# Performance work log

Hardware: AMD Instinct MI355X
Metric: run time of the kernel (lower is better)

The kernel has to match this reference:

```python
import jax, jax.numpy as jnp
import numpy as np

NP, NC, F, H = 50000, 10000, 128, 256
E_ANNO, E_LINK, E_PPI, NPAIR = 250000, 100000, 500000, 4096


def _sage(x_src, x_dst, src, dst, Wl, b, Wr):
    # PyG SAGEConv(aggr='mean'): lin_l(mean of gathered neighbor feats) + lin_r(x_dst)
    n_dst = x_dst.shape[0]
    agg = jax.ops.segment_sum(x_src[src], dst, num_segments=n_dst)
    cnt = jax.ops.segment_sum(jnp.ones((src.shape[0], 1), x_src.dtype), dst, num_segments=n_dst)
    mean = agg / jnp.maximum(cnt, 1.0)  # isolated dst nodes get 0
    return mean @ Wl.T + b + x_dst @ Wr.T


def setup_inputs():
    key = jax.random.key(0)
    ks = iter(jax.random.split(key, 64))
    s = 0.05
    inp = {}
    inp['x_protein'] = jax.random.normal(next(ks), (NP, F), jnp.float32)
    inp['x_class'] = jax.random.normal(next(ks), (NC, F), jnp.float32)
    for layer, din, dout in [('a', F, H), ('b', H, F)]:
        for rel in ['annop', 'annon', 'link', 'ppi']:
            inp[f'{layer}_{rel}_Wl'] = jax.random.normal(next(ks), (dout, din), jnp.float32) * s
            inp[f'{layer}_{rel}_b'] = jax.random.normal(next(ks), (dout,), jnp.float32) * s
            inp[f'{layer}_{rel}_Wr'] = jax.random.normal(next(ks), (dout, din), jnp.float32) * s
    inp['lin_W'] = jax.random.normal(next(ks), (1, 2 * F), jnp.float32) * s
    inp['lin_b'] = jnp.zeros((1,), jnp.float32)
    inp['annop_src'] = jax.random.randint(next(ks), (E_ANNO,), 0, NP)
    inp['annop_dst'] = jax.random.randint(next(ks), (E_ANNO,), 0, NC)
    inp['annon_src'] = jax.random.randint(next(ks), (E_ANNO,), 0, NP)
    inp['annon_dst'] = jax.random.randint(next(ks), (E_ANNO,), 0, NC)
    inp['link_src'] = jax.random.randint(next(ks), (E_LINK,), 0, NC)
    inp['link_dst'] = jax.random.randint(next(ks), (E_LINK,), 0, NC)
    inp['ppi_src'] = jax.random.randint(next(ks), (E_PPI,), 0, NP)
    inp['ppi_dst'] = jax.random.randint(next(ks), (E_PPI,), 0, NP)
    inp['mask'] = jax.random.randint(next(ks), (NPAIR, 2), 0, NP)
    return inp


def reference(x_protein, x_class,
              a_annop_Wl, a_annop_b, a_annop_Wr,
              a_annon_Wl, a_annon_b, a_annon_Wr,
              a_link_Wl, a_link_b, a_link_Wr,
              a_ppi_Wl, a_ppi_b, a_ppi_Wr,
              b_annop_Wl, b_annop_b, b_annop_Wr,
              b_annon_Wl, b_annon_b, b_annon_Wr,
              b_link_Wl, b_link_b, b_link_Wr,
              b_ppi_Wl, b_ppi_b, b_ppi_Wr,
              lin_W, lin_b,
              annop_src, annop_dst, annon_src, annon_dst,
              link_src, link_dst, ppi_src, ppi_dst, mask):
    # Layer 1 (HeteroConv aggregates per dst node type with sum)
    hc = (_sage(x_protein, x_class, annop_src, annop_dst, a_annop_Wl, a_annop_b, a_annop_Wr)
          + _sage(x_protein, x_class, annon_src, annon_dst, a_annon_Wl, a_annon_b, a_annon_Wr)
          + _sage(x_class, x_class, link_src, link_dst, a_link_Wl, a_link_b, a_link_Wr))
    hp = _sage(x_protein, x_protein, ppi_src, ppi_dst, a_ppi_Wl, a_ppi_b, a_ppi_Wr)
    hc = jax.nn.relu(hc)
    hp = jax.nn.relu(hp)
    # Layer 2
    hp2 = _sage(hp, hp, ppi_src, ppi_dst, b_ppi_Wl, b_ppi_b, b_ppi_Wr)
    # (class outputs of layer 2 are computed in the original but unused for the head)
    hc2 = (_sage(hp, hc, annop_src, annop_dst, b_annop_Wl, b_annop_b, b_annop_Wr)
           + _sage(hp, hc, annon_src, annon_dst, b_annon_Wl, b_annon_b, b_annon_Wr)
           + _sage(hc, hc, link_src, link_dst, b_link_Wl, b_link_b, b_link_Wr))
    del hc2
    # Pair readout: mask.T -> rows of protein indices; original detaches p1, p2
    p1 = jax.lax.stop_gradient(hp2[mask[:, 0]])
    p2 = jax.lax.stop_gradient(hp2[mask[:, 1]])
    h = jnp.concatenate((p1, p2), axis=1)  # [NPAIR, 2F]
    return jax.nn.sigmoid(h @ lin_W.T + lin_b)
```

## Files before the change

### kernel.cpp

```cpp
#include <hip/hip_runtime.h>
#include <math.h>

#define NPROT 50000
#define NPROT_PAD 50048
#define EPPI 500000
#define NPAIR 4096
#define SLAB 64

typedef __attribute__((ext_vector_type(8))) __bf16 bf16x8;
typedef __attribute__((ext_vector_type(4))) __bf16 bf16x4;
typedef __attribute__((ext_vector_type(4))) float floatx4;

__global__ void k_prep(const float* __restrict__ x,
                       const float* __restrict__ Wl, const float* __restrict__ Wr,
                       const float* __restrict__ linW, const float* __restrict__ linb,
                       const float* __restrict__ bWl, const float* __restrict__ bWr,
                       const float* __restrict__ bb,
                       __bf16* __restrict__ Xb, __bf16* __restrict__ Bw,
                       float* __restrict__ P, float* __restrict__ biasC,
                       int* __restrict__ cnt) {
    __shared__ float sP[10];
    int b = blockIdx.x, t = threadIdx.x;
    if (b < 6250) {
        int i = b * 256 + t;
        int row = i >> 5, k4 = (i & 31) << 2;
        float4 v = *(const float4*)(x + (size_t)row * 128 + k4);
        bf16x4 o; o[0] = (__bf16)v.x; o[1] = (__bf16)v.y; o[2] = (__bf16)v.z; o[3] = (__bf16)v.w;
        *(bf16x4*)(Xb + (size_t)row * 128 + k4) = o;
    } else if (b < 6506) {
        int idx = (b - 6250) * 256 + t;
        int h = idx >> 8, k = idx & 255;
        float v = (k < 128) ? Wl[h * 128 + k] : Wr[h * 128 + (k - 128)];
        Bw[idx] = (__bf16)v;
    } else if (b < 6762) {
        int h = b - 6506;
        int lane = t & 63, wave = t >> 6;
        float v1 = 0, v2 = 0, u1 = 0, u2 = 0, c = 0;
        if (t < 128) {
            float w1 = linW[t], w2 = linW[128 + t];
            float wl = bWl[t * 256 + h], wr = bWr[t * 256 + h];
            v1 = w1 * wl; v2 = w2 * wl; u1 = w1 * wr; u2 = w2 * wr;
            if (h == 0) c = (w1 + w2) * bb[t];
        }
#pragma unroll
        for (int m = 1; m < 64; m <<= 1) {
            v1 += __shfl_xor(v1, m, 64); v2 += __shfl_xor(v2, m, 64);
            u1 += __shfl_xor(u1, m, 64); u2 += __shfl_xor(u2, m, 64);
            c  += __shfl_xor(c, m, 64);
        }
        if (lane == 0 && wave < 2) {
            sP[wave * 5 + 0] = v1; sP[wave * 5 + 1] = v2;
            sP[wave * 5 + 2] = u1; sP[wave * 5 + 3] = u2;
            sP[wave * 5 + 4] = c;
        }
        __syncthreads();
        if (t == 0) {
            P[h * 4 + 0] = sP[0] + sP[5]; P[h * 4 + 1] = sP[1] + sP[6];
            P[h * 4 + 2] = sP[2] + sP[7]; P[h * 4 + 3] = sP[3] + sP[8];
            if (h == 0) *biasC = linb[0] + sP[4] + sP[9];
        }
    } else {
        int i = (b - 6762) * 256 + t;
        if (i < NPROT) cnt[i] = 0;
    }
}

__global__ void k_link(const int* __restrict__ src, const int* __restrict__ dst,
                       int* __restrict__ cnt, int* __restrict__ slab) {
    int e = blockIdx.x * 256 + threadIdx.x;
    if (e < EPPI) {
        int d = dst[e];
        int pos = atomicAdd(&cnt[d], 1);
        if (pos < SLAB) slab[(size_t)d * SLAB + pos] = src[e];
    }
}

__global__ void k_agg(const __bf16* __restrict__ Xb, const int* __restrict__ cnt,
                      const int* __restrict__ slab, __bf16* __restrict__ Am) {
    int wave = threadIdx.x >> 6, lane = threadIdx.x & 63;
    int q = lane >> 4, sl = lane & 15;
    int node = blockIdx.x * 16 + wave * 4 + q;
    if (node >= NPROT) return;
    float a[8];
#pragma unroll
    for (int e8 = 0; e8 < 8; e8++) a[e8] = 0.f;
    const __bf16* base = Xb + (size_t)sl * 8;
    int c = cnt[node];
    if (c > SLAB) c = SLAB;
    const int* sp = slab + (size_t)node * SLAB;
    int j = 0;
    for (; j + 8 <= c; j += 8) {
        int4 sa = *(const int4*)(sp + j);
        int4 sb = *(const int4*)(sp + j + 4);
        bf16x8 v0 = *(const bf16x8*)(base + (size_t)sa.x * 128);
        bf16x8 v1 = *(const bf16x8*)(base + (size_t)sa.y * 128);
        bf16x8 v2 = *(const bf16x8*)(base + (size_t)sa.z * 128);
        bf16x8 v3 = *(const bf16x8*)(base + (size_t)sa.w * 128);
        bf16x8 v4 = *(const bf16x8*)(base + (size_t)sb.x * 128);
        bf16x8 v5 = *(const bf16x8*)(base + (size_t)sb.y * 128);
        bf16x8 v6 = *(const bf16x8*)(base + (size_t)sb.z * 128);
        bf16x8 v7 = *(const bf16x8*)(base + (size_t)sb.w * 128);
#pragma unroll
        for (int e8 = 0; e8 < 8; e8++)
            a[e8] += (float)v0[e8] + (float)v1[e8] + (float)v2[e8] + (float)v3[e8]
                   + (float)v4[e8] + (float)v5[e8] + (float)v6[e8] + (float)v7[e8];
    }
    for (; j < c; j++) {
        int s = sp[j];
        bf16x8 v = *(const bf16x8*)(base + (size_t)s * 128);
#pragma unroll
        for (int e8 = 0; e8 < 8; e8++) a[e8] += (float)v[e8];
    }
    float iv = 1.0f / (float)(c > 1 ? c : 1);
    bf16x8 o;
#pragma unroll
    for (int e8 = 0; e8 < 8; e8++) o[e8] = (__bf16)(a[e8] * iv);
    *(bf16x8*)(Am + (size_t)node * 128 + sl * 8) = o;
}

__global__ __launch_bounds__(256) void k_gemm(const __bf16* __restrict__ Am,
                                              const __bf16* __restrict__ Xb,
                                              const __bf16* __restrict__ Bw,
                                              const float* __restrict__ ab,
                                              const float* __restrict__ P,
                                              float* __restrict__ y) {
    __shared__ __bf16 Bs[2048 * 8];
    int tid = threadIdx.x;
    int half = blockIdx.x & 1;
    int rb   = blockIdx.x >> 1;
    int wave = tid >> 6, lane = tid & 63;
    int r = lane & 15, quad = lane >> 4;
    int row0 = rb * 128 + wave * 32;

    bf16x8 afrag[2][8];
#pragma unroll
    for (int g = 0; g < 2; g++) {
        const __bf16* mp = Am + (size_t)(row0 + g * 16 + r) * 128 + quad * 8;
        const __bf16* op = Xb + (size_t)(row0 + g * 16 + r) * 128 + quad * 8;
#pragma unroll
        for (int kk = 0; kk < 4; kk++) {
            afrag[g][kk]     = *(const bf16x8*)(mp + kk * 32);
            afrag[g][4 + kk] = *(const bf16x8*)(op + kk * 32);
        }
    }

    float part[2][4][4] = {{{0.f}}};

    for (int cc = 0; cc < 2; cc++) {
        int chunk = half * 2 + cc;
        if (cc) __syncthreads();
#pragma unroll
        for (int jj = 0; jj < 8; jj++) {
            int g = jj * 256 + tid;
            int gr = g & 15, gq = (g >> 4) & 3;
            int gkk = (g >> 6) & 7;
            int gt = g >> 9;
            const __bf16* src = Bw + (size_t)(chunk * 64 + gt * 16 + gr) * 256 + gkk * 32 + gq * 8;
            __builtin_amdgcn_global_load_lds(
                (const __attribute__((address_space(1))) void*)src,
                (__attribute__((address_space(3))) void*)(Bs + (size_t)g * 8),
                16, 0, 0);
        }
        __syncthreads();

        floatx4 acc[2][4];
#pragma unroll
        for (int g = 0; g < 2; g++)
#pragma unroll
            for (int t = 0; t < 4; t++) acc[g][t] = (floatx4){0.f, 0.f, 0.f, 0.f};
#pragma unroll
        for (int kk = 0; kk < 8; kk++) {
#pragma unroll
            for (int t = 0; t < 4; t++) {
                bf16x8 bf = *(const bf16x8*)(Bs + (size_t)((t * 8 + kk) * 64 + lane) * 8);
                acc[0][t] = __builtin_amdgcn_mfma_f32_16x16x32_bf16(afrag[0][kk], bf, acc[0][t], 0, 0, 0);
                acc[1][t] = __builtin_amdgcn_mfma_f32_16x16x32_bf16(afrag[1][kk], bf, acc[1][t], 0, 0, 0);
            }
        }

#pragma unroll
        for (int t = 0; t < 4; t++) {
            int col = chunk * 64 + t * 16 + r;
            float bias = ab[col];
            float4 pv = *(const float4*)(P + col * 4);
#pragma unroll
            for (int g = 0; g < 2; g++)
#pragma unroll
                for (int rr = 0; rr < 4; rr++) {
                    float h = acc[g][t][rr] + bias;
                    h = h > 0.f ? h : 0.f;
                    part[g][rr][0] += h * pv.x; part[g][rr][1] += h * pv.y;
                    part[g][rr][2] += h * pv.z; part[g][rr][3] += h * pv.w;
                }
        }
    }

#pragma unroll
    for (int m = 1; m < 16; m <<= 1)
#pragma unroll
        for (int g = 0; g < 2; g++)
#pragma unroll
            for (int rr = 0; rr < 4; rr++)
#pragma unroll
                for (int j = 0; j < 4; j++)
                    part[g][rr][j] += __shfl_xor(part[g][rr][j], m, 64);
    if (r == 0) {
#pragma unroll
        for (int g = 0; g < 2; g++)
#pragma unroll
            for (int rr = 0; rr < 4; rr++) {
                int row = row0 + g * 16 + quad * 4 + rr;
                float4 o;
                o.x = part[g][rr][0]; o.y = part[g][rr][1];
                o.z = part[g][rr][2]; o.w = part[g][rr][3];
                *(float4*)(y + (size_t)row * 8 + half * 4) = o;
            }
    }
}

__global__ void k_head(const int* __restrict__ mask, const int* __restrict__ cnt,
                       const int* __restrict__ slab, const float* __restrict__ y,
                       const float* __restrict__ biasC, float* __restrict__ out) {
    int tid = blockIdx.x * 256 + threadIdx.x;
    int p = tid >> 1, side = tid & 1;
    float res = 0.f;
    if (p < NPAIR) {
        int node = mask[p * 2 + side];
        int c = cnt[node];
        if (c > SLAB) c = SLAB;
        const int* sp = slab + (size_t)node * SLAB;
        float s = 0.f;
        int j = 0;
        for (; j + 4 <= c; j += 4) {
            int4 sa = *(const int4*)(sp + j);
            s += y[(size_t)sa.x * 8 + side] + y[(size_t)sa.x * 8 + 4 + side];
            s += y[(size_t)sa.y * 8 + side] + y[(size_t)sa.y * 8 + 4 + side];
            s += y[(size_t)sa.z * 8 + side] + y[(size_t)sa.z * 8 + 4 + side];
            s += y[(size_t)sa.w * 8 + side] + y[(size_t)sa.w * 8 + 4 + side];
        }
        for (; j < c; j++) {
            int si = sp[j];
            s += y[(size_t)si * 8 + side] + y[(size_t)si * 8 + 4 + side];
        }
        float iv = 1.0f / (float)(c > 1 ? c : 1);
        res = s * iv + y[(size_t)node * 8 + 2 + side] + y[(size_t)node * 8 + 6 + side];
    }
    float other = __shfl_xor(res, 1, 64);
    if (p < NPAIR && side == 0) {
        float z = res + other + *biasC;
        out[p] = 1.f / (1.f + expf(-z));
    }
}

extern "C" void kernel_launch(void* const* d_in, const int* in_sizes, int n_in,
                              void* d_out, int out_size, void* d_ws, size_t ws_size,
                              hipStream_t stream) {
    const float* x_protein = (const float*)d_in[0];
    const float* a_ppi_Wl  = (const float*)d_in[11];
    const float* a_ppi_b   = (const float*)d_in[12];
    const float* a_ppi_Wr  = (const float*)d_in[13];
    const float* b_ppi_Wl  = (const float*)d_in[23];
    const float* b_ppi_b   = (const float*)d_in[24];
    const float* b_ppi_Wr  = (const float*)d_in[25];
    const float* lin_W     = (const float*)d_in[26];
    const float* lin_b     = (const float*)d_in[27];
    const int* ppi_src     = (const int*)d_in[34];
    const int* ppi_dst     = (const int*)d_in[35];
    const int* mask        = (const int*)d_in[36];
    float* out = (float*)d_out;

    char* ws = (char*)d_ws;
    size_t o = 0;
    auto alloc = [&](size_t n) -> char* {
        char* r = ws + o;
        o = (o + n + 511) & ~(size_t)511;
        return r;
    };
    int*    cnt    = (int*)alloc((size_t)NPROT * 4);
    int*    slab   = (int*)alloc((size_t)NPROT * SLAB * 4);
    __bf16* Xb     = (__bf16*)alloc((size_t)NPROT_PAD * 128 * 2);
    __bf16* Am     = (__bf16*)alloc((size_t)NPROT_PAD * 128 * 2);
    __bf16* Bw     = (__bf16*)alloc(256 * 256 * 2);
    float*  P      = (float*)alloc(256 * 4 * 4);
    float*  biasC  = (float*)alloc(4);
    float*  y      = (float*)alloc((size_t)NPROT_PAD * 8 * 4);
    (void)ws_size;

    k_prep<<<6958, 256, 0, stream>>>(x_protein, a_ppi_Wl, a_ppi_Wr, lin_W, lin_b,
                                     b_ppi_Wl, b_ppi_Wr, b_ppi_b,
                                     Xb, Bw, P, biasC, cnt);
    k_link<<<(EPPI + 255) / 256, 256, 0, stream>>>(ppi_src, ppi_dst, cnt, slab);
    k_agg<<<(NPROT + 15) / 16, 256, 0, stream>>>(Xb, cnt, slab, Am);
    k_gemm<<<782, 256, 0, stream>>>(Am, Xb, Bw, a_ppi_b, P, y);
    k_head<<<(2 * NPAIR + 255) / 256, 256, 0, stream>>>(mask, cnt, slab, y, biasC, out);
}
```

Measured before the change: 226.3 us.

## Drop LDS staging in GEMM, read weights from global and cover all columns per block

The GEMM kernel no longer stages weight chunks into LDS through global_load_lds with barriers. Each 128-thread block now handles 64 rows across all four 64-column chunks, reading B fragments straight from global memory, which the L2 cache should serve because the weight matrix is small. Because one block now sums every output column, the y buffer shrinks from 8 to 4 floats per node and the head kernel reads half as many values per neighbour. This removes LDS traffic and sync overhead but adds repeated global loads of B per wave and loop overhead from the unroll-1 chunk loop.

```diff
diff --git a/kernel.cpp b/kernel.cpp
--- a/kernel.cpp
+++ b/kernel.cpp
@@ -118,19 +118,16 @@
     *(bf16x8*)(Am + (size_t)node * 128 + sl * 8) = o;
 }
 
-__global__ __launch_bounds__(256) void k_gemm(const __bf16* __restrict__ Am,
+__global__ __launch_bounds__(128) void k_gemm(const __bf16* __restrict__ Am,
                                               const __bf16* __restrict__ Xb,
                                               const __bf16* __restrict__ Bw,
                                               const float* __restrict__ ab,
                                               const float* __restrict__ P,
                                               float* __restrict__ y) {
-    __shared__ __bf16 Bs[2048 * 8];
     int tid = threadIdx.x;
-    int half = blockIdx.x & 1;
-    int rb   = blockIdx.x >> 1;
     int wave = tid >> 6, lane = tid & 63;
     int r = lane & 15, quad = lane >> 4;
-    int row0 = rb * 128 + wave * 32;
+    int row0 = blockIdx.x * 64 + wave * 32;
 
     bf16x8 afrag[2][8];
 #pragma unroll
@@ -146,33 +143,19 @@
 
     float part[2][4][4] = {{{0.f}}};
 
-    for (int cc = 0; cc < 2; cc++) {
-        int chunk = half * 2 + cc;
-        if (cc) __syncthreads();
-#pragma unroll
-        for (int jj = 0; jj < 8; jj++) {
-            int g = jj * 256 + tid;
-            int gr = g & 15, gq = (g >> 4) & 3;
-            int gkk = (g >> 6) & 7;
-            int gt = g >> 9;
-            const __bf16* src = Bw + (size_t)(chunk * 64 + gt * 16 + gr) * 256 + gkk * 32 + gq * 8;
-            __builtin_amdgcn_global_load_lds(
-                (const __attribute__((address_space(1))) void*)src,
-                (__attribute__((address_space(3))) void*)(Bs + (size_t)g * 8),
-                16, 0, 0);
-        }
-        __syncthreads();
-
+#pragma unroll 1
+    for (int chunk = 0; chunk < 4; chunk++) {
         floatx4 acc[2][4];
 #pragma unroll
         for (int g = 0; g < 2; g++)
 #pragma unroll
             for (int t = 0; t < 4; t++) acc[g][t] = (floatx4){0.f, 0.f, 0.f, 0.f};
+        const __bf16* bp = Bw + (size_t)(chunk * 64 + r) * 256 + quad * 8;
 #pragma unroll
         for (int kk = 0; kk < 8; kk++) {
 #pragma unroll
             for (int t = 0; t < 4; t++) {
-                bf16x8 bf = *(const bf16x8*)(Bs + (size_t)((t * 8 + kk) * 64 + lane) * 8);
+                bf16x8 bf = *(const bf16x8*)(bp + (size_t)t * 16 * 256 + kk * 32);
                 acc[0][t] = __builtin_amdgcn_mfma_f32_16x16x32_bf16(afrag[0][kk], bf, acc[0][t], 0, 0, 0);
                 acc[1][t] = __builtin_amdgcn_mfma_f32_16x16x32_bf16(afrag[1][kk], bf, acc[1][t], 0, 0, 0);
             }
@@ -213,7 +196,7 @@
                 float4 o;
                 o.x = part[g][rr][0]; o.y = part[g][rr][1];
                 o.z = part[g][rr][2]; o.w = part[g][rr][3];
-                *(float4*)(y + (size_t)row * 8 + half * 4) = o;
+                *(float4*)(y + (size_t)row * 4) = o;
             }
     }
 }
@@ -233,17 +216,17 @@
         int j = 0;
         for (; j + 4 <= c; j += 4) {
             int4 sa = *(const int4*)(sp + j);
-            s += y[(size_t)sa.x * 8 + side] + y[(size_t)sa.x * 8 + 4 + side];
-            s += y[(size_t)sa.y * 8 + side] + y[(size_t)sa.y * 8 + 4 + side];
-            s += y[(size_t)sa.z * 8 + side] + y[(size_t)sa.z * 8 + 4 + side];
-            s += y[(size_t)sa.w * 8 + side] + y[(size_t)sa.w * 8 + 4 + side];
+            s += y[(size_t)sa.x * 4 + side];
+            s += y[(size_t)sa.y * 4 + side];
+            s += y[(size_t)sa.z * 4 + side];
+            s += y[(size_t)sa.w * 4 + side];
         }
         for (; j < c; j++) {
             int si = sp[j];
-            s += y[(size_t)si * 8 + side] + y[(size_t)si * 8 + 4 + side];
+            s += y[(size_t)si * 4 + side];
         }
         float iv = 1.0f / (float)(c > 1 ? c : 1);
-        res = s * iv + y[(size_t)node * 8 + 2 + side] + y[(size_t)node * 8 + 6 + side];
+        res = s * iv + y[(size_t)node * 4 + 2 + side];
     }
     float other = __shfl_xor(res, 1, 64);
     if (p < NPAIR && side == 0) {
@@ -283,7 +266,7 @@
     __bf16* Bw     = (__bf16*)alloc(256 * 256 * 2);
     float*  P      = (float*)alloc(256 * 4 * 4);
     float*  biasC  = (float*)alloc(4);
-    float*  y      = (float*)alloc((size_t)NPROT_PAD * 8 * 4);
+    float*  y      = (float*)alloc((size_t)NPROT_PAD * 4 * 4);
     (void)ws_size;
 
     k_prep<<<6958, 256, 0, stream>>>(x_protein, a_ppi_Wl, a_ppi_Wr, lin_W, lin_b,
@@ -291,6 +274,6 @@
                                      Xb, Bw, P, biasC, cnt);
     k_link<<<(EPPI + 255) / 256, 256, 0, stream>>>(ppi_src, ppi_dst, cnt, slab);
     k_agg<<<(NPROT + 15) / 16, 256, 0, stream>>>(Xb, cnt, slab, Am);
-    k_gemm<<<782, 256, 0, stream>>>(Am, Xb, Bw, a_ppi_b, P, y);
+    k_gemm<<<NPROT_PAD / 64, 128, 0, stream>>>(Am, Xb, Bw, a_ppi_b, P, y);
     k_head<<<(2 * NPAIR + 255) / 256, 256, 0, stream>>>(mask, cnt, slab, y, biasC, out);
 }
```

After: 240.1 us. +6.1%, slower.
